# Kernel optimization log

Measured on AMD Instinct MI355X. Metric: run time of the kernel, lower is better.

Reference implementation:

```python
import jax, jax.numpy as jnp
import numpy as np

N_FFT = 2048
HOP = 441
DIM = 512


def _hann(n_fft):
    # torch.hann_window (periodic): 0.5*(1 - cos(2*pi*n/N))
    n = jnp.arange(n_fft, dtype=jnp.float32)
    return 0.5 * (1.0 - jnp.cos(2.0 * jnp.pi * n / n_fft))


def setup_inputs() -> dict:
    key = jax.random.key(0)
    k1, k2, k3 = jax.random.split(key, 3)
    x = jax.random.normal(k1, (4, 2, 1323000), dtype=jnp.float32)
    W_enc = 1e-4 * jax.random.normal(k2, (DIM, N_FFT), dtype=jnp.float32)
    W_dec = 1e-4 * jax.random.normal(k3, (N_FFT, DIM), dtype=jnp.float32)
    return {"x": x, "W_enc": W_enc, "W_dec": W_dec, "length": 1323000}


def reference(x, W_enc, W_dec, length):
    b, c, L = x.shape
    pad = N_FFT // 2
    window = _hann(N_FFT)

    # ---- encode ----
    xp = jnp.pad(x, ((0, 0), (0, 0), (pad, pad)), mode="reflect")  # (b,c,L+n_fft)
    Lp = xp.shape[-1]
    t = (Lp - N_FFT) // HOP + 1  # num frames
    idx = jnp.arange(t)[:, None] * HOP + jnp.arange(N_FFT)[None, :]  # (t, n)
    frames = xp[..., idx] * window  # (b,c,t,n) -- the overlapping unfold buffer
    feat = jnp.einsum("bctn,mn->bctm", frames, W_enc)  # (b,c,t,dim)

    # ---- decode ----
    rec = jnp.einsum("bctm,nm->bctn", feat, W_dec)  # (b,c,t,n)
    L2 = N_FFT + (t - 1) * HOP
    # overlap-add (F.fold) over merged (b*c) rows
    out = jnp.zeros((b * c, L2), dtype=rec.dtype)
    out = out.at[:, idx].add(rec.reshape(b * c, t, N_FFT))
    # window normalization (second fold in the original)
    win_norm = jnp.zeros((L2,), dtype=rec.dtype)
    win_norm = win_norm.at[idx].add(jnp.broadcast_to(window, (t, N_FFT)))
    out = out / jnp.clip(win_norm, 1e-8)
    out = out.reshape(b, c, L2)[..., pad:pad + length]
    return out
```

## Files before the change

kernel.cpp:

```cpp
#include <hip/hip_runtime.h>
#include <stdint.h>

typedef unsigned short u16;
typedef unsigned int u32;
typedef __attribute__((ext_vector_type(8))) short short8;
typedef __attribute__((ext_vector_type(4))) float f32x4;

#define L_IN   1323000
#define PAD    1024
#define HOP    441
#define T_FR   3001
#define M_ROWS 24008
#define NB     3008
#define RPAD   448
#define K1E    2240
#define K2     2560
#define W_2PI_N 3.0679615757712823e-3f

__device__ __forceinline__ u16 f2bf(float f) {
  union { float f; u32 u; } v; v.f = f;
  u32 r = v.u + 0x7FFFu + ((v.u >> 16) & 1u);
  return (u16)(r >> 16);
}

__device__ __forceinline__ void gload16(const void* g, void* l) {
  __builtin_amdgcn_global_load_lds(
      (const __attribute__((address_space(1))) u32*)g,
      (__attribute__((address_space(3))) u32*)l, 16, 0, 0);
}

__device__ __forceinline__ void tile_from_bid(int bid, int& m0, int& n0) {
  int g = (bid & 7) * 94 + (bid >> 3);
  m0 = (g >> 2) * 128;
  n0 = (g & 3) * 128;
}

__global__ void prep_all(const float* __restrict__ x,
                         const float* __restrict__ W_enc, const float* __restrict__ W_dec,
                         u16* __restrict__ xb, u16* __restrict__ wh2,
                         u16* __restrict__ b2, float* __restrict__ zeros) {
  int stride = gridDim.x * blockDim.x;
  int tid0 = blockIdx.x * blockDim.x + threadIdx.x;
  for (int idx = tid0; idx < 64; idx += stride) zeros[idx] = 0.f;
  for (int idx = tid0; idx < 8 * NB * RPAD; idx += stride) {
    int bc = idx / (NB * RPAD);
    int rem = idx - bc * (NB * RPAD);
    int u = rem / RPAD;
    int r = rem - u * RPAD;
    int s = HOP * u + r - PAD;
    int ja = s < 0 ? -s : s;
    int jb = 2 * L_IN - 2 - ja;
    int jr = ja < jb ? ja : jb;
    xb[idx] = f2bf(x[(size_t)bc * L_IN + jr]);
  }
  for (int idx = tid0; idx < 512 * K1E; idx += stride) {
    int m = idx / K1E;
    int k = idx - m * K1E;
    int j = k / RPAD;
    int r = k - j * RPAD;
    int n = HOP * j + r;
    float v = 0.f;
    if (r < HOP && n < 2048)
      v = (0.5f - 0.5f * cosf(W_2PI_N * (float)n)) * W_enc[m * 2048 + n];
    wh2[idx] = f2bf(v);
  }
  for (int idx = tid0; idx < 512 * K2; idx += stride) {
    int r = idx / K2;
    int k = idx - r * K2;
    int j = k >> 9;
    int m = k & 511;
    int n = HOP * j + r;
    float v = (r < HOP && n < 2048) ? W_dec[n * 512 + m] : 0.f;
    b2[idx] = f2bf(v);
  }
}

__device__ __forceinline__ void mfma_tile(const u16* sA, const u16* sB, f32x4 acc[4][4],
                                          int lane, int wr, int wc) {
  const int lr = lane & 15;
  const int hi = lane >> 4;
  #pragma unroll
  for (int ks = 0; ks < 2; ++ks) {
    const int off = (((ks * 4 + hi) ^ (lr & 7)) << 3);
    short8 af[4], bg[4];
    #pragma unroll
    for (int f = 0; f < 4; ++f)
      af[f] = *(const short8*)(sA + (wr + f * 16 + lr) * 64 + off);
    #pragma unroll
    for (int f = 0; f < 4; ++f)
      bg[f] = *(const short8*)(sB + (wc + f * 16 + lr) * 64 + off);
    #pragma unroll
    for (int mf = 0; mf < 4; ++mf)
      #pragma unroll
      for (int nf = 0; nf < 4; ++nf)
        acc[mf][nf] = __builtin_amdgcn_mfma_f32_16x16x32_bf16(af[mf], bg[nf], acc[mf][nf], 0, 0, 0);
  }
}


__global__ __launch_bounds__(256, 2)
void gemm_enc(const u16* __restrict__ xb, const u16* __restrict__ wh2,
              u16* __restrict__ featb) {
  __shared__ u16 sA[128 * 64];
  __shared__ u16 sB[128 * 64];
  const int tid = threadIdx.x;
  const int lane = tid & 63;
  const int w = tid >> 6;
  int m0, n0;
  tile_from_bid(blockIdx.x, m0, n0);
  const int colsw = (((lane & 7) ^ ((lane >> 3) & 7)) << 3);

  const u16* bsrc[4];
  const u16* asrc[4];
  #pragma unroll
  for (int i = 0; i < 4; ++i) {
    int row = (i * 4 + w) * 8 + (lane >> 3);
    bsrc[i] = wh2 + (size_t)(n0 + row) * K1E + colsw;
    int rg = m0 + row;
    int rgc = rg < M_ROWS ? rg : (M_ROWS - 1);
    int bc = rgc / T_FR;
    int t  = rgc - bc * T_FR;
    asrc[i] = xb + ((size_t)bc * NB + t) * RPAD + colsw;
  }

  f32x4 acc[4][4];
  #pragma unroll
  for (int a = 0; a < 4; ++a)
    #pragma unroll
    for (int b = 0; b < 4; ++b) acc[a][b] = f32x4{0.f, 0.f, 0.f, 0.f};

  const int wr = (w >> 1) * 64, wc = (w & 1) * 64;

  for (int kc = 0; kc < K1E; kc += 64) {
    __syncthreads();
    #pragma unroll
    for (int i = 0; i < 4; ++i)
      gload16(bsrc[i] + kc, &sB[(i * 4 + w) * 512]);
    #pragma unroll
    for (int i = 0; i < 4; ++i)
      gload16(asrc[i] + kc, &sA[(i * 4 + w) * 512]);
    __syncthreads();
    mfma_tile(sA, sB, acc, lane, wr, wc);
  }

  #pragma unroll
  for (int mf = 0; mf < 4; ++mf) {
    #pragma unroll
    for (int e = 0; e < 4; ++e) {
      int rg = m0 + wr + mf * 16 + ((lane >> 4) << 2) + e;
      if (rg < M_ROWS) {
        #pragma unroll
        for (int nf = 0; nf < 4; ++nf) {
          int cg = n0 + wc + nf * 16 + (lane & 15);
          featb[(size_t)rg * 512 + cg] = f2bf(acc[mf][nf][e]);
        }
      }
    }
  }
}


__global__ __launch_bounds__(256, 2)
void gemm_dec(const u16* __restrict__ featb, const u16* __restrict__ b2,
              const u16* __restrict__ zeros, float* __restrict__ out) {
  __shared__ u16 sA[128 * 64];
  __shared__ u16 sB[128 * 64];
  const int tid = threadIdx.x;
  const int lane = tid & 63;
  const int w = tid >> 6;
  const int m0 = blockIdx.y * 128;
  const int n0 = blockIdx.x * 128;
  const int colsw = (((lane & 7) ^ ((lane >> 3) & 7)) << 3);

  const u16* bsrc[4];
  const u16* fsrc[4];
  int qiv[4];
  unsigned vmask = 0;
  #pragma unroll
  for (int i = 0; i < 4; ++i) {
    int row = (i * 4 + w) * 8 + (lane >> 3);
    bsrc[i] = b2 + (size_t)(n0 + row) * K2 + colsw;
    int rg = m0 + row;
    int rgc = rg < M_ROWS ? rg : (M_ROWS - 1);
    int bc = rgc / T_FR;
    int qi = rgc - bc * T_FR;
    if (rg < M_ROWS) vmask |= 1u << i;
    qiv[i] = qi;
    fsrc[i] = featb + (size_t)(bc * T_FR + qi + 2) * 512 + colsw;
  }

  f32x4 acc[4][4];
  #pragma unroll
  for (int a = 0; a < 4; ++a)
    #pragma unroll
    for (int b = 0; b < 4; ++b) acc[a][b] = f32x4{0.f, 0.f, 0.f, 0.f};

  const int wr = (w >> 1) * 64, wc = (w & 1) * 64;

  for (int kc = 0; kc < K2; kc += 64) {
    int jt = kc >> 9;
    __syncthreads();
    #pragma unroll
    for (int i = 0; i < 4; ++i)
      gload16(bsrc[i] + kc, &sB[(i * 4 + w) * 512]);
    #pragma unroll
    for (int i = 0; i < 4; ++i) {
      int t = qiv[i] + 2 - jt;
      bool ok = ((vmask >> i) & 1) && (t >= 0) && (t <= 3000);
      const u16* pa = ok ? (fsrc[i] + kc - 1024 * jt) : (zeros + colsw);
      gload16(pa, &sA[(i * 4 + w) * 512]);
    }
    __syncthreads();
    mfma_tile(sA, sB, acc, lane, wr, wc);
  }

  const int lr16 = lane & 15;
  float hh[4][5];
  float rnfull[4];
  int cgv[4];
  #pragma unroll
  for (int nf = 0; nf < 4; ++nf) {
    int cg = n0 + wc + nf * 16 + lr16;
    cgv[nf] = cg;
    float s = 0.f;
    #pragma unroll
    for (int j = 0; j < 5; ++j) {
      int n = HOP * j + cg;
      float h = (cg < HOP && n < 2048) ? (0.5f - 0.5f * cosf(W_2PI_N * (float)n)) : 0.f;
      hh[nf][j] = h;
      s += h;
    }
    rnfull[nf] = 1.f / fmaxf(s, 1e-8f);
  }

  #pragma unroll
  for (int mf = 0; mf < 4; ++mf) {
    #pragma unroll
    for (int e = 0; e < 4; ++e) {
      int rg = m0 + wr + mf * 16 + ((lane >> 4) << 2) + e;
      if (rg < M_ROWS) {
        int bc = rg / T_FR;
        int qi = rg - bc * T_FR;
        int ib = HOP * qi - 142;
        bool interior = (qi >= 2) && (qi <= 2998);
        #pragma unroll
        for (int nf = 0; nf < 4; ++nf) {
          if (cgv[nf] < HOP) {
            int oi = ib + cgv[nf];
            if (oi >= 0 && oi < L_IN) {
              float rn;
              if (interior) {
                rn = rnfull[nf];
              } else {
                float s = 0.f;
                #pragma unroll
                for (int j = 0; j < 5; ++j)
                  if ((unsigned)(qi + 2 - j) <= 3000u) s += hh[nf][j];
                rn = 1.f / fmaxf(s, 1e-8f);
              }
              out[(size_t)bc * L_IN + oi] = acc[mf][nf][e] * rn;
            }
          }
        }
      }
    }
  }
}


extern "C" void kernel_launch(void* const* d_in, const int* in_sizes, int n_in,
                              void* d_out, int out_size, void* d_ws, size_t ws_size,
                              hipStream_t stream) {
  const float* x     = (const float*)d_in[0];
  const float* W_enc = (const float*)d_in[1];
  const float* W_dec = (const float*)d_in[2];
  float* out = (float*)d_out;
  char* ws = (char*)d_ws;

  u16* xb = (u16*)d_out;

  u16*   wh2   = (u16*)  (ws + 0);
  u16*   b2    = (u16*)  (ws + 2293760);
  u16*   featb = (u16*)  (ws + 4915200);
  float* zeros = (float*)(ws + 29499392);

  prep_all<<<2048, 256, 0, stream>>>(x, W_enc, W_dec, xb, wh2, b2, zeros);
  gemm_enc<<<752, 256, 0, stream>>>(xb, wh2, featb);
  gemm_dec<<<dim3(4, 188), 256, 0, stream>>>(featb, b2, (const u16*)zeros, out);
}
```

Measured before the change: 153.4 us.

## Rewrite decoder GEMM as 256x256 tile with double-buffered phased LDS pipeline

Replaces the 128x128, 4-wave decoder GEMM with a 256x256-tile, 8-wave kernel. Global-to-LDS loads for the next K chunk are double-buffered and interleaved with four MFMA phases, using explicit vmcnt waits, barriers and s_setprio. This is meant to hide load latency and raise data reuse per block. In exchange the grid shrinks to 188 blocks, fewer than the CU count, and each block uses about 128KB of LDS, which may leave CUs idle and limit occupancy.

```diff
diff --git a/kernel.cpp b/kernel.cpp
--- a/kernel.cpp
+++ b/kernel.cpp
@@ -15,6 +15,7 @@
 #define RPAD   448
 #define K1E    2240
 #define K2     2560
+#define NT2    40
 #define W_2PI_N 3.0679615757712823e-3f
 
 __device__ __forceinline__ u16 f2bf(float f) {
@@ -97,7 +98,6 @@
   }
 }
 
-
 __global__ __launch_bounds__(256, 2)
 void gemm_enc(const u16* __restrict__ xb, const u16* __restrict__ wh2,
               u16* __restrict__ featb) {
@@ -159,68 +159,131 @@
   }
 }
 
-
-__global__ __launch_bounds__(256, 2)
-void gemm_dec(const u16* __restrict__ featb, const u16* __restrict__ b2,
-              const u16* __restrict__ zeros, float* __restrict__ out) {
-  __shared__ u16 sA[128 * 64];
-  __shared__ u16 sB[128 * 64];
+template<int P>
+__device__ __forceinline__ void phase_mfma(const u16* cA, const short8 bfr[4][2],
+                                           f32x4 acc[8][4], int wm, int lr, int hi) {
+  short8 a0[2], a1[2];
+  #pragma unroll
+  for (int ks = 0; ks < 2; ++ks) {
+    const int ch = ((((ks << 2) | hi) ^ (lr & 7)) << 3);
+    a0[ks] = *(const short8*)(cA + wm * 8192 + ((2 * P) * 16 + lr) * 64 + ch);
+    a1[ks] = *(const short8*)(cA + wm * 8192 + ((2 * P + 1) * 16 + lr) * 64 + ch);
+  }
+  __builtin_amdgcn_s_setprio(1);
+  #pragma unroll
+  for (int ks = 0; ks < 2; ++ks)
+    #pragma unroll
+    for (int nf = 0; nf < 4; ++nf) {
+      acc[2 * P][nf]     = __builtin_amdgcn_mfma_f32_16x16x32_bf16(a0[ks], bfr[nf][ks], acc[2 * P][nf], 0, 0, 0);
+      acc[2 * P + 1][nf] = __builtin_amdgcn_mfma_f32_16x16x32_bf16(a1[ks], bfr[nf][ks], acc[2 * P + 1][nf], 0, 0, 0);
+    }
+  __builtin_amdgcn_s_setprio(0);
+}
+
+__global__ __launch_bounds__(512, 2)
+void gemm_dec8(const u16* __restrict__ featb, const u16* __restrict__ b2,
+               const u16* __restrict__ zeros, float* __restrict__ out) {
+  __shared__ u16 sA[32768];
+  __shared__ u16 sB[32768];
   const int tid = threadIdx.x;
   const int lane = tid & 63;
   const int w = tid >> 6;
-  const int m0 = blockIdx.y * 128;
-  const int n0 = blockIdx.x * 128;
+  const int wm = w >> 2;
+  const int wn = w & 3;
+  const int lr = lane & 15;
+  const int hi = lane >> 4;
+  const int n0 = blockIdx.x * 256;
+  const int m0 = blockIdx.y * 256;
   const int colsw = (((lane & 7) ^ ((lane >> 3) & 7)) << 3);
 
-  const u16* bsrc[4];
-  const u16* fsrc[4];
-  int qiv[4];
-  unsigned vmask = 0;
-  #pragma unroll
-  for (int i = 0; i < 4; ++i) {
-    int row = (i * 4 + w) * 8 + (lane >> 3);
-    bsrc[i] = b2 + (size_t)(n0 + row) * K2 + colsw;
-    int rg = m0 + row;
-    int rgc = rg < M_ROWS ? rg : (M_ROWS - 1);
-    int bc = rgc / T_FR;
-    int qi = rgc - bc * T_FR;
-    if (rg < M_ROWS) vmask |= 1u << i;
-    qiv[i] = qi;
-    fsrc[i] = featb + (size_t)(bc * T_FR + qi + 2) * 512 + colsw;
-  }
-
-  f32x4 acc[4][4];
-  #pragma unroll
-  for (int a = 0; a < 4; ++a)
+  int offA[2][2]; int qiv[2][2]; unsigned amask = 0;
+  int offB[2][2];
+  #pragma unroll
+  for (int h = 0; h < 2; ++h)
+    #pragma unroll
+    for (int l = 0; l < 2; ++l) {
+      int rowA = 128 * h + 8 * (w + 8 * l) + (lane >> 3);
+      int rg = m0 + rowA;
+      int rgc = rg < M_ROWS ? rg : (M_ROWS - 1);
+      int bc = rgc / T_FR;
+      int qi = rgc - bc * T_FR;
+      if (rg < M_ROWS) amask |= 1u << (h * 2 + l);
+      qiv[h][l] = qi;
+      offA[h][l] = (bc * T_FR + qi + 2) * 512 + colsw;
+      int rowB = n0 + 128 * h + 8 * (w + 8 * l) + (lane >> 3);
+      offB[h][l] = rowB * K2 + colsw;
+    }
+
+  f32x4 acc[8][4];
+  #pragma unroll
+  for (int a = 0; a < 8; ++a)
     #pragma unroll
     for (int b = 0; b < 4; ++b) acc[a][b] = f32x4{0.f, 0.f, 0.f, 0.f};
 
-  const int wr = (w >> 1) * 64, wc = (w & 1) * 64;
-
-  for (int kc = 0; kc < K2; kc += 64) {
+  auto stB = [&](int kc, int bufi, int h) {
+    gload16(b2 + offB[h][0] + kc, sB + bufi * 16384 + h * 8192 + w * 512);
+    gload16(b2 + offB[h][1] + kc, sB + bufi * 16384 + h * 8192 + (w + 8) * 512);
+  };
+  auto stA = [&](int kc, int bufi, int l) {
     int jt = kc >> 9;
-    __syncthreads();
-    #pragma unroll
-    for (int i = 0; i < 4; ++i)
-      gload16(bsrc[i] + kc, &sB[(i * 4 + w) * 512]);
-    #pragma unroll
-    for (int i = 0; i < 4; ++i) {
-      int t = qiv[i] + 2 - jt;
-      bool ok = ((vmask >> i) & 1) && (t >= 0) && (t <= 3000);
-      const u16* pa = ok ? (fsrc[i] + kc - 1024 * jt) : (zeros + colsw);
-      gload16(pa, &sA[(i * 4 + w) * 512]);
-    }
-    __syncthreads();
-    mfma_tile(sA, sB, acc, lane, wr, wc);
-  }
-
-  const int lr16 = lane & 15;
+    #pragma unroll
+    for (int h = 0; h < 2; ++h) {
+      int tt = qiv[h][l] + 2 - jt;
+      bool ok = ((amask >> (h * 2 + l)) & 1) && tt >= 0 && tt <= 3000;
+      const u16* pa = ok ? (featb + offA[h][l] + kc - 1024 * jt) : (zeros + colsw);
+      gload16(pa, sA + bufi * 16384 + h * 8192 + (w + 8 * l) * 512);
+    }
+  };
+
+  stB(0, 0, 0); stB(0, 0, 1); stA(0, 0, 0); stA(0, 0, 1);
+
+  #pragma unroll 1
+  for (int t = 0; t < NT2; ++t) {
+    const int buf = t & 1, nxt = buf ^ 1;
+    const int kcn = (t + 1) * 64;
+    const u16* cA = sA + buf * 16384;
+    const u16* cB = sB + buf * 16384;
+    if (t < NT2 - 1) {
+      stB(kcn, nxt, 0);
+      asm volatile("s_waitcnt vmcnt(4)\n\ts_barrier" ::: "memory");
+    } else {
+      asm volatile("s_waitcnt vmcnt(2)\n\ts_barrier" ::: "memory");
+    }
+    short8 bfr[4][2];
+    #pragma unroll
+    for (int nf = 0; nf < 4; ++nf)
+      #pragma unroll
+      for (int ks = 0; ks < 2; ++ks) {
+        int rb = (wn & 1) * 64 + nf * 16 + lr;
+        bfr[nf][ks] = *(const short8*)(cB + (wn >> 1) * 8192 + rb * 64 +
+                                       ((((ks << 2) | hi) ^ (lr & 7)) << 3));
+      }
+    phase_mfma<0>(cA, bfr, acc, wm, lr, hi);
+    asm volatile("s_barrier" ::: "memory");
+    if (t < NT2 - 1) stB(kcn, nxt, 1);
+    asm volatile("s_barrier" ::: "memory");
+    phase_mfma<1>(cA, bfr, acc, wm, lr, hi);
+    asm volatile("s_barrier" ::: "memory");
+    if (t < NT2 - 1) {
+      stA(kcn, nxt, 0);
+      asm volatile("s_waitcnt vmcnt(6)\n\ts_barrier" ::: "memory");
+    } else {
+      asm volatile("s_waitcnt vmcnt(0)\n\ts_barrier" ::: "memory");
+    }
+    phase_mfma<2>(cA, bfr, acc, wm, lr, hi);
+    asm volatile("s_barrier" ::: "memory");
+    if (t < NT2 - 1) stA(kcn, nxt, 1);
+    asm volatile("s_barrier" ::: "memory");
+    phase_mfma<3>(cA, bfr, acc, wm, lr, hi);
+    asm volatile("s_barrier" ::: "memory");
+  }
+
   float hh[4][5];
   float rnfull[4];
   int cgv[4];
   #pragma unroll
   for (int nf = 0; nf < 4; ++nf) {
-    int cg = n0 + wc + nf * 16 + lr16;
+    int cg = n0 + wn * 64 + nf * 16 + lr;
     cgv[nf] = cg;
     float s = 0.f;
     #pragma unroll
@@ -234,10 +297,10 @@
   }
 
   #pragma unroll
-  for (int mf = 0; mf < 4; ++mf) {
+  for (int mf = 0; mf < 8; ++mf) {
     #pragma unroll
     for (int e = 0; e < 4; ++e) {
-      int rg = m0 + wr + mf * 16 + ((lane >> 4) << 2) + e;
+      int rg = m0 + wm * 128 + mf * 16 + (hi << 2) + e;
       if (rg < M_ROWS) {
         int bc = rg / T_FR;
         int qi = rg - bc * T_FR;
@@ -286,5 +349,5 @@
 
   prep_all<<<2048, 256, 0, stream>>>(x, W_enc, W_dec, xb, wh2, b2, zeros);
   gemm_enc<<<752, 256, 0, stream>>>(xb, wh2, featb);
-  gemm_dec<<<dim3(4, 188), 256, 0, stream>>>(featb, b2, (const u16*)zeros, out);
-}
+  gemm_dec8<<<dim3(2, 94), 512, 0, stream>>>(featb, b2, (const u16*)zeros, out);
+}
```

Measured after the change: 206.1 us. 1.34x slower.
